# Performance work log

Hardware: AMD Instinct MI355X
Metric: run time of the kernel (lower is better)

## Reference

```python
import jax, jax.numpy as jnp
import numpy as np

TEMPERATURE = 0.1
N = 8192   # batch*views (4096 ids, 2 views)
D = 128


def setup_inputs() -> dict:
    key = jax.random.key(0)
    z = jax.random.normal(key, (N, D), dtype=jnp.float32)
    # two views per sample: ids 0..N/2-1 repeated, so every row has a positive
    indexes = jnp.tile(jnp.arange(N // 2, dtype=jnp.int64), 2)
    return {"z": z, "indexes": indexes}


def reference(z, indexes):
    # L2-normalize features (single process: gathered_z == z)
    zn = z / jnp.linalg.norm(z, axis=-1, keepdims=True)
    # [N, N] exp-similarity
    sim = jnp.exp(jnp.einsum('if,jf->ij', zn, zn) / TEMPERATURE)
    eq = indexes[:, None] == indexes[None, :]          # same id
    eye = jnp.eye(indexes.shape[0], dtype=bool)        # self-similarity
    pos_mask = eq & ~eye                                # positives, diag zeroed
    neg_mask = ~eq                                      # negatives
    pos = jnp.sum(sim * pos_mask, axis=1)
    neg = jnp.sum(sim * neg_mask, axis=1)
    loss = -jnp.mean(jnp.log(pos / (pos + neg)))
    return loss
```

## Files before the change

kernel.cpp:

```cpp
#include <hip/hip_runtime.h>
#include <hip/hip_bf16.h>


constexpr int N = 8192;
constexpr int D = 128;
constexpr float SCALE = 14.4269504088896341f;

typedef short bf16x8 __attribute__((ext_vector_type(8)));
typedef float f32x4 __attribute__((ext_vector_type(4)));

#if __has_builtin(__builtin_amdgcn_exp2f)
#define EXP2(x) __builtin_amdgcn_exp2f(x)
#else
#define EXP2(x) exp2f(x)
#endif

static __device__ __forceinline__ unsigned short f2bf(float x) {
  __hip_bfloat16 h = __float2bfloat16(x);
  unsigned short u;
  __builtin_memcpy(&u, &h, 2);
  return u;
}
static __device__ __forceinline__ float bf2f(unsigned short u) {
  unsigned int x = ((unsigned int)u) << 16;
  float f;
  __builtin_memcpy(&f, &x, 4);
  return f;
}
static __device__ __forceinline__ void gload_lds16(const void* g, void* l) {
  __builtin_amdgcn_global_load_lds(
      (const __attribute__((address_space(1))) unsigned int*)g,
      (__attribute__((address_space(3))) unsigned int*)l, 16, 0, 0);
}

__global__ __launch_bounds__(256) void simclr_prep(const float* __restrict__ z,
                                                   unsigned short* __restrict__ znb,
                                                   unsigned short* __restrict__ znbs,
                                                   float* __restrict__ selfe,
                                                   float* __restrict__ poslog) {
  const int row = blockIdx.x * 4 + (threadIdx.x >> 6);
  const int par = row ^ (N / 2);
  const int lane = threadIdx.x & 63;
  const float2 v = *(const float2*)(z + row * D + lane * 2);
  const float2 b = *(const float2*)(z + par * D + lane * 2);
  float ss = v.x * v.x + v.y * v.y;
  float sb = b.x * b.x + b.y * b.y;
  float dp = v.x * b.x + v.y * b.y;
#pragma unroll
  for (int m = 1; m < 64; m <<= 1) {
    ss += __shfl_xor(ss, m);
    sb += __shfl_xor(sb, m);
    dp += __shfl_xor(dp, m);
  }
  const float rn = rsqrtf(ss);
  const float a0 = v.x * rn, a1 = v.y * rn;
  const unsigned short u0 = f2bf(a0), u1 = f2bf(a1);
  const unsigned short s0 = f2bf(a0 * SCALE), s1 = f2bf(a1 * SCALE);
  *(unsigned int*)(znb + row * D + lane * 2) = (unsigned int)u0 | ((unsigned int)u1 << 16);
  *(unsigned int*)(znbs + row * D + lane * 2) = (unsigned int)s0 | ((unsigned int)s1 << 16);
  float sa = bf2f(s0) * bf2f(u0) + bf2f(s1) * bf2f(u1);
#pragma unroll
  for (int m = 1; m < 64; m <<= 1) sa += __shfl_xor(sa, m);
  if (lane == 0) {
    selfe[row] = EXP2(sa);
    poslog[row] = 10.0f * dp * rsqrtf(ss * sb);
  }
}

__global__ __launch_bounds__(512)
__attribute__((amdgpu_waves_per_eu(4, 4)))
void simclr_sim(const unsigned short* __restrict__ znb,
                const unsigned short* __restrict__ znbs,
                float* __restrict__ partials) {
  __shared__ unsigned short lb[2][64 * 128];

  const int bi = blockIdx.x;
  const int RB = (bi >> 5) << 8;
  const int CB = (bi & 31) << 8;
  const int tid = threadIdx.x;
  const int lane = tid & 63;
  const int w = tid >> 6;
  const int l15 = lane & 15, l4 = lane >> 4;

  bf16x8 afrag[2][4];
#pragma unroll
  for (int rt = 0; rt < 2; ++rt)
#pragma unroll
    for (int s = 0; s < 4; ++s)
      afrag[rt][s] =
          *(const bf16x8*)(znbs + (RB + w * 32 + rt * 16 + l15) * D + s * 32 + l4 * 8);

  float dpart[8];
#pragma unroll
  for (int k = 0; k < 8; ++k) dpart[k] = 0.f;

#define STAGE(buf_, cc_)                                                        \
  {                                                                             \
    _Pragma("unroll") for (int i = 0; i < 2; ++i) {                             \
      const int rr = (w * 2 + i) * 4 + l4;                                      \
      const unsigned short* g =                                                 \
          znb + (CB + (cc_) * 64 + rr) * D + ((l15 ^ (rr & 7)) << 3);           \
      gload_lds16(g, (char*)lb[buf_] + (w * 2 + i) * 1024);                     \
    }                                                                           \
  }

  STAGE(0, 0);
  __syncthreads();

  int buf = 0;
  for (int cc = 0; cc < 4; ++cc) {
    if (cc < 3) STAGE(buf ^ 1, cc + 1);
    const char* lbc = (const char*)lb[buf];
#pragma unroll
    for (int jt = 0; jt < 4; ++jt) {
      const int jr = jt * 16 + l15;
      const int swz = (jr & 7) << 4;
      bf16x8 bfrag[4];
#pragma unroll
      for (int s = 0; s < 4; ++s)
        bfrag[s] = *(const bf16x8*)(lbc + jr * 256 + ((s * 64 + l4 * 16) ^ swz));
      f32x4 acc[2];
#pragma unroll
      for (int rt = 0; rt < 2; ++rt) acc[rt] = f32x4{0.f, 0.f, 0.f, 0.f};
#pragma unroll
      for (int s = 0; s < 4; ++s)
#pragma unroll
        for (int rt = 0; rt < 2; ++rt)
          acc[rt] = __builtin_amdgcn_mfma_f32_16x16x32_bf16(afrag[rt][s], bfrag[s],
                                                            acc[rt], 0, 0, 0);
#pragma unroll
      for (int rt = 0; rt < 2; ++rt)
#pragma unroll
        for (int r = 0; r < 4; ++r) dpart[rt * 4 + r] += EXP2(acc[rt][r]);
    }
    __syncthreads();
    buf ^= 1;
  }
#undef STAGE

#pragma unroll
  for (int m = 1; m < 16; m <<= 1)
#pragma unroll
    for (int k = 0; k < 8; ++k) dpart[k] += __shfl_xor(dpart[k], m);

  if (l15 == 0) {
    float* pp = partials + (bi & 31) * N + RB + w * 32 + l4 * 4;
#pragma unroll
    for (int rt = 0; rt < 2; ++rt)
#pragma unroll
      for (int r = 0; r < 4; ++r) pp[rt * 16 + r] = dpart[rt * 4 + r];
  }
}

__global__ __launch_bounds__(256) void simclr_rowloss(const float* __restrict__ partials,
                                                      const float* __restrict__ selfe,
                                                      const float* __restrict__ poslog,
                                                      float* __restrict__ bsum) {
  const int tid = threadIdx.x;
  const int i = blockIdx.x * 256 + tid;
  float d = -selfe[i];
#pragma unroll
  for (int cb = 0; cb < 32; ++cb) d += partials[cb * N + i];
  float s = logf(d) - poslog[i];
#pragma unroll
  for (int m = 1; m < 64; m <<= 1) s += __shfl_xor(s, m);
  __shared__ float acc[4];
  if ((tid & 63) == 0) acc[tid >> 6] = s;
  __syncthreads();
  if (tid == 0) bsum[blockIdx.x] = acc[0] + acc[1] + acc[2] + acc[3];
}

__global__ __launch_bounds__(64) void simclr_final(const float* __restrict__ bsum,
                                                   float* __restrict__ out) {
  const int tid = threadIdx.x;
  float s = (tid < 32) ? bsum[tid] : 0.f;
#pragma unroll
  for (int m = 1; m < 64; m <<= 1) s += __shfl_xor(s, m);
  if (tid == 0) out[0] = s * (1.0f / N);
}

extern "C" void kernel_launch(void* const* d_in, const int* in_sizes, int n_in,
                              void* d_out, int out_size, void* d_ws, size_t ws_size,
                              hipStream_t stream) {
  const float* z = (const float*)d_in[0];
  float* out = (float*)d_out;

  float* partials = (float*)d_ws;
  float* selfe = partials + 32 * N;
  float* poslog = selfe + N;
  float* bsum = poslog + N;
  unsigned short* znb = (unsigned short*)(bsum + 64);
  unsigned short* znbs = znb + N * D;

  simclr_prep<<<N / 4, 256, 0, stream>>>(z, znb, znbs, selfe, poslog);
  simclr_sim<<<(N / 256) * (N / 256), 512, 0, stream>>>(znb, znbs, partials);
  simclr_rowloss<<<N / 256, 256, 0, stream>>>(partials, selfe, poslog, bsum);
  simclr_final<<<1, 64, 0, stream>>>(bsum, out);
}
```

Baseline: 86.09 us.

## Exploit similarity-matrix symmetry by computing only upper-triangular tiles

The sim kernel now makes blocks below the diagonal return at once. Each off-diagonal tile also produces column sums of its exp-similarities, reduced across waves in shared memory and written into the mirrored partials slot. This cuts the MFMA and exp work of the N×N similarity pass roughly in half. The cost is extra shuffles and LDS traffic per tile, and diagonal tiles skew the workload. The result also relies on near-symmetry of the scaled-bf16 by unscaled-bf16 product, so rounding can differ slightly between mirrored entries.

```diff
diff --git a/kernel.cpp b/kernel.cpp
--- a/kernel.cpp
+++ b/kernel.cpp
@@ -72,15 +72,20 @@
 void simclr_sim(const unsigned short* __restrict__ znb,
                 const unsigned short* __restrict__ znbs,
                 float* __restrict__ partials) {
+  const int bi = blockIdx.x;
+  const int I = bi >> 5, J = bi & 31;
+  if (J < I) return;
+
   __shared__ unsigned short lb[2][64 * 128];
-
-  const int bi = blockIdx.x;
-  const int RB = (bi >> 5) << 8;
-  const int CB = (bi & 31) << 8;
+  __shared__ float colacc[8][256];
+
+  const int RB = I << 8;
+  const int CB = J << 8;
   const int tid = threadIdx.x;
   const int lane = tid & 63;
   const int w = tid >> 6;
   const int l15 = lane & 15, l4 = lane >> 4;
+  const bool offdiag = (I != J);
 
   bf16x8 afrag[2][4];
 #pragma unroll
@@ -128,10 +133,20 @@
         for (int rt = 0; rt < 2; ++rt)
           acc[rt] = __builtin_amdgcn_mfma_f32_16x16x32_bf16(afrag[rt][s], bfrag[s],
                                                             acc[rt], 0, 0, 0);
+      float s8 = 0.f;
 #pragma unroll
       for (int rt = 0; rt < 2; ++rt)
 #pragma unroll
-        for (int r = 0; r < 4; ++r) dpart[rt * 4 + r] += EXP2(acc[rt][r]);
+        for (int r = 0; r < 4; ++r) {
+          const float e = EXP2(acc[rt][r]);
+          dpart[rt * 4 + r] += e;
+          s8 += e;
+        }
+      if (offdiag) {
+        s8 += __shfl_xor(s8, 16);
+        s8 += __shfl_xor(s8, 32);
+        if (l4 == 0) colacc[w][cc * 64 + jt * 16 + l15] = s8;
+      }
     }
     __syncthreads();
     buf ^= 1;
@@ -144,11 +159,18 @@
     for (int k = 0; k < 8; ++k) dpart[k] += __shfl_xor(dpart[k], m);
 
   if (l15 == 0) {
-    float* pp = partials + (bi & 31) * N + RB + w * 32 + l4 * 4;
+    float* pp = partials + J * N + RB + w * 32 + l4 * 4;
 #pragma unroll
     for (int rt = 0; rt < 2; ++rt)
 #pragma unroll
       for (int r = 0; r < 4; ++r) pp[rt * 16 + r] = dpart[rt * 4 + r];
+  }
+
+  if (offdiag && tid < 256) {
+    float cs = 0.f;
+#pragma unroll
+    for (int w2 = 0; w2 < 8; ++w2) cs += colacc[w2][tid];
+    partials[I * N + CB + tid] = cs;
   }
 }
 
@@ -193,7 +215,7 @@
   unsigned short* znbs = znb + N * D;
 
   simclr_prep<<<N / 4, 256, 0, stream>>>(z, znb, znbs, selfe, poslog);
-  simclr_sim<<<(N / 256) * (N / 256), 512, 0, stream>>>(znb, znbs, partials);
+  simclr_sim<<<32 * 32, 512, 0, stream>>>(znb, znbs, partials);
   simclr_rowloss<<<N / 256, 256, 0, stream>>>(partials, selfe, poslog, bsum);
   simclr_final<<<1, 64, 0, stream>>>(bsum, out);
 }
```

Result: slower. 105.9 us (+23.1%).
